# Optimization experiments

Measured on AMD Instinct MI355X. Metric: run time of the kernel, lower is better.

## Reference

```python
import jax, jax.numpy as jnp
import numpy as np

N = 20000        # total nodes in batched graph
E = 160000       # edges (avg in-degree 8)
D_IN = 512
D_OUT = 512
MAX_DEG = 10
BN_EPS = 1e-5


def setup_inputs() -> dict:
    key = jax.random.key(0)
    ks = jax.random.split(key, 8)
    feats = jax.random.normal(ks[0], (N, D_IN), dtype=jnp.float32)
    src = jax.random.randint(ks[1], (E,), 0, N)
    dst = jax.random.randint(ks[2], (E,), 0, N)
    # Wl[d], bl[d]: lins_l for degree d (d>=1); Wl[0] is never used since h==0 for deg-0 nodes.
    # Wr[0], bl[0] play the role of lin_zero_deg; Wr[d] (d>=1) are the bias-free lins_r.
    Wl = jax.random.normal(ks[3], (MAX_DEG + 1, D_IN, D_OUT), dtype=jnp.float32) * 0.02
    Wr = jax.random.normal(ks[4], (MAX_DEG + 1, D_IN, D_OUT), dtype=jnp.float32) * 0.02
    bl = jax.random.normal(ks[5], (MAX_DEG + 1, D_OUT), dtype=jnp.float32) * 0.02
    gamma = jnp.ones((D_OUT,), dtype=jnp.float32)
    beta = jnp.zeros((D_OUT,), dtype=jnp.float32)
    return {"feats": feats, "src": src, "dst": dst, "Wl": Wl, "Wr": Wr,
            "bl": bl, "gamma": gamma, "beta": beta}


def reference(feats, src, dst, Wl, Wr, bl, gamma, beta):
    # 1) neighbor sum: h[v] = sum_{(u->v) in E} feats[u]   (fn.copy_u + fn.sum)
    h = jax.ops.segment_sum(feats[src], dst, num_segments=N)  # [N, D_IN]
    # in-degrees, clamped to max_degree
    deg = jnp.clip(jax.ops.segment_sum(jnp.ones((E,), dtype=jnp.int32), dst,
                                       num_segments=N), 0, MAX_DEG)  # [N]
    # 2) degree-bucketed linears, vectorized over the 11 buckets then gathered per node.
    #    out[n] = h[n] @ Wl[deg[n]] + feats[n] @ Wr[deg[n]] + bl[deg[n]]
    #    deg==0 nodes have h==0, so this reduces to lin_zero_deg(feats) = feats@Wr[0]+bl[0].
    Hl = jnp.einsum('ni,dio->dno', h, Wl)      # [11, N, D_OUT]
    Hr = jnp.einsum('ni,dio->dno', feats, Wr)  # [11, N, D_OUT]
    out = (Hl + Hr + bl[:, None, :])[deg, jnp.arange(N)]  # [N, D_OUT]
    # 3) batchnorm (training mode: batch stats, biased variance)
    mean = out.mean(axis=0)
    var = out.var(axis=0)
    out = (out - mean) * jax.lax.rsqrt(var + BN_EPS) * gamma + beta
    # 4) max aggregation over graph with self loops (fn.copy_u + fn.max)
    self_ids = jnp.arange(N)
    src_s = jnp.concatenate([src, self_ids])
    dst_s = jnp.concatenate([dst, self_ids])
    out = jax.ops.segment_max(out[src_s], dst_s, num_segments=N)  # [N, D_OUT]
    return out
```

## Files before the change

### kernel.cpp

```cpp
#include <hip/hip_runtime.h>
#include <hip/hip_bf16.h>
#include <stdint.h>

#define N_NODES 20000
#define N_EDGES 160000
#define DIN 512
#define DOUT 512
#define NBUCKET 11
#define KDIM 1024
#define MAXTILES 168
#define BN_EPS 1e-5f
#define CAP 64
#define CAST_BLOCKS (N_NODES / 4)
#define WT_BLOCKS ((KDIM / 32) * (DOUT / 32) * NBUCKET)
#define BUCKET_BLOCKS ((N_NODES + 255) / 256)

typedef float f32x4 __attribute__((ext_vector_type(4)));
typedef __attribute__((ext_vector_type(8))) __bf16 bf16x8;

static __device__ __forceinline__ unsigned short f2bf(float f) {
    union { float f; unsigned u; } v; v.f = f;
    unsigned r = v.u + 0x7FFFu + ((v.u >> 16) & 1u);
    return (unsigned short)(r >> 16);
}
static __device__ __forceinline__ float bflo(unsigned p) {
    union { unsigned u; float f; } v; v.u = p << 16; return v.f;
}
static __device__ __forceinline__ float bfhi(unsigned p) {
    union { unsigned u; float f; } v; v.u = p & 0xFFFF0000u; return v.f;
}
static __device__ __forceinline__ unsigned packbf(float lo, float hi) {
    return (unsigned)f2bf(lo) | ((unsigned)f2bf(hi) << 16);
}

static __device__ __forceinline__ void gload_lds16(const unsigned short* g, unsigned short* l) {
    __builtin_amdgcn_global_load_lds(
        (const __attribute__((address_space(1))) unsigned int*)g,
        (__attribute__((address_space(3))) unsigned int*)l, 16, 0, 0);
}

__global__ void k_scatter(const int* __restrict__ src, const int* __restrict__ dst,
                          int* __restrict__ cursor, int* __restrict__ eidx2) {
    int e = blockIdx.x * 256 + threadIdx.x;
    if (e >= N_EDGES) return;
    int v = dst[e];
    int slot = atomicAdd(&cursor[v], 1);
    if (slot < CAP) eidx2[v * CAP + slot] = src[e];
}

__global__ __launch_bounds__(256)
void k_prep(const float* __restrict__ feats, const float* __restrict__ Wl,
            const float* __restrict__ Wr, const int* __restrict__ cursor,
            unsigned short* __restrict__ X, unsigned short* __restrict__ Wt,
            int* __restrict__ bucket_cnt, int* __restrict__ bucket_nodes) {
    int b = blockIdx.x;
    int t = threadIdx.x;
    if (b < CAST_BLOCKS) {
        int n = b * 4 + (t >> 6);
        int col = (t & 63) * 8;
        f32x4 a = *(const f32x4*)(feats + (size_t)n * DIN + col);
        f32x4 c = *(const f32x4*)(feats + (size_t)n * DIN + col + 4);
        uint4 p;
        p.x = packbf(a[0], a[1]); p.y = packbf(a[2], a[3]);
        p.z = packbf(c[0], c[1]); p.w = packbf(c[2], c[3]);
        *(uint4*)(X + (size_t)n * KDIM + DIN + col) = p;
        return;
    }
    if (b < CAST_BLOCKS + WT_BLOCKS) {
        __shared__ float tile[32][33];
        int idx = b - CAST_BLOCKS;
        int d = idx / (32 * 16);
        int rem = idx % (32 * 16);
        int k0 = (rem & 31) * 32;
        int n0 = (rem >> 5) * 32;
        int c = t & 31, r0 = t >> 5;
        const float* srcp = (k0 < DIN) ? (Wl + (size_t)d * DIN * DOUT)
                                       : (Wr + (size_t)d * DIN * DOUT - (size_t)DIN * DOUT);
        for (int rr = 0; rr < 4; ++rr) {
            int r = r0 + rr * 8;
            tile[r][c] = srcp[(size_t)(k0 + r) * DOUT + n0 + c];
        }
        __syncthreads();
        for (int rr = 0; rr < 4; ++rr) {
            int r = r0 + rr * 8;
            Wt[((size_t)d * DOUT + n0 + r) * KDIM + k0 + c] = f2bf(tile[c][r]);
        }
        return;
    }
    __shared__ int lhist[NBUCKET];
    __shared__ int lbase[NBUCKET];
    if (t < NBUCKET) lhist[t] = 0;
    __syncthreads();
    int v = (b - CAST_BLOCKS - WT_BLOCKS) * 256 + t;
    int d = -1, slot = 0;
    if (v < N_NODES) {
        d = min(cursor[v], NBUCKET - 1);
        slot = atomicAdd(&lhist[d], 1);
    }
    __syncthreads();
    if (t < NBUCKET && lhist[t] > 0) lbase[t] = atomicAdd(&bucket_cnt[t], lhist[t]);
    __syncthreads();
    if (v < N_NODES) bucket_nodes[d * N_NODES + lbase[d] + slot] = v;
}

__global__ __launch_bounds__(256)
void k_build_x(const int* __restrict__ eidx2, const int* __restrict__ cursor,
               unsigned short* __restrict__ X) {
    int n = blockIdx.x * 4 + (threadIdx.x >> 6);
    int col = (threadIdx.x & 63) * 8;
    const int* adj = eidx2 + (size_t)n * CAP;
    int e = min(cursor[n], CAP);
    float acc[8] = {0,0,0,0,0,0,0,0};
    int i = 0;
    for (; i + 3 < e; i += 4) {
        int u0 = adj[i], u1 = adj[i+1], u2 = adj[i+2], u3 = adj[i+3];
        uint4 p0 = *(const uint4*)(X + (size_t)u0 * KDIM + DIN + col);
        uint4 p1 = *(const uint4*)(X + (size_t)u1 * KDIM + DIN + col);
        uint4 p2 = *(const uint4*)(X + (size_t)u2 * KDIM + DIN + col);
        uint4 p3 = *(const uint4*)(X + (size_t)u3 * KDIM + DIN + col);
        acc[0] += bflo(p0.x) + bflo(p1.x) + bflo(p2.x) + bflo(p3.x);
        acc[1] += bfhi(p0.x) + bfhi(p1.x) + bfhi(p2.x) + bfhi(p3.x);
        acc[2] += bflo(p0.y) + bflo(p1.y) + bflo(p2.y) + bflo(p3.y);
        acc[3] += bfhi(p0.y) + bfhi(p1.y) + bfhi(p2.y) + bfhi(p3.y);
        acc[4] += bflo(p0.z) + bflo(p1.z) + bflo(p2.z) + bflo(p3.z);
        acc[5] += bfhi(p0.z) + bfhi(p1.z) + bfhi(p2.z) + bfhi(p3.z);
        acc[6] += bflo(p0.w) + bflo(p1.w) + bflo(p2.w) + bflo(p3.w);
        acc[7] += bfhi(p0.w) + bfhi(p1.w) + bfhi(p2.w) + bfhi(p3.w);
    }
    for (; i < e; ++i) {
        int u = adj[i];
        uint4 p = *(const uint4*)(X + (size_t)u * KDIM + DIN + col);
        acc[0] += bflo(p.x); acc[1] += bfhi(p.x); acc[2] += bflo(p.y); acc[3] += bfhi(p.y);
        acc[4] += bflo(p.z); acc[5] += bfhi(p.z); acc[6] += bflo(p.w); acc[7] += bfhi(p.w);
    }
    uint4 o;
    o.x = packbf(acc[0], acc[1]); o.y = packbf(acc[2], acc[3]);
    o.z = packbf(acc[4], acc[5]); o.w = packbf(acc[6], acc[7]);
    *(uint4*)(X + (size_t)n * KDIM + col) = o;
}

__global__ __launch_bounds__(256)
void k_gemm(const unsigned short* __restrict__ X, const unsigned short* __restrict__ Wt,
            const int* __restrict__ bucket_nodes, const int* __restrict__ bucket_cnt,
            const float* __restrict__ bl, unsigned short* __restrict__ out_pre,
            float* __restrict__ bn_sum, float* __restrict__ bn_sumsq) {
    int idx = blockIdx.x;
    int d = -1, m0 = 0, accum = 0, cnt = 0;
    for (int b = 0; b < NBUCKET; ++b) {
        int c = bucket_cnt[b];
        int nt = (c + 127) >> 7;
        if (d < 0 && idx < accum + nt) { d = b; m0 = (idx - accum) * 128; cnt = c; }
        accum += nt;
    }
    if (d < 0) return;
    int n0 = blockIdx.y * 128;

    __shared__ __align__(16) unsigned short As[128 * 64];
    __shared__ __align__(16) unsigned short Bs[128 * 64];
    __shared__ int ridS[128];
    __shared__ float colsum[128], colsq[128];

    int t = threadIdx.x;
    if (t < 128) {
        int gm = m0 + t;
        ridS[t] = (gm < cnt) ? bucket_nodes[d * N_NODES + gm] : -1;
        colsum[t] = 0.f; colsq[t] = 0.f;
    }
    __syncthreads();

    int lane = t & 63, w = t >> 6;
    int r = lane >> 3;
    int s = lane & 7;
    int sg = s ^ r;

    const unsigned short* gA[4];
    const unsigned short* gB[4];
    unsigned short* lA[4];
    unsigned short* lB[4];
#pragma unroll
    for (int j = 0; j < 4; ++j) {
        int row = w * 32 + j * 8 + r;
        int rid = max(ridS[row], 0);
        gA[j] = X + (size_t)rid * KDIM + sg * 8;
        gB[j] = Wt + ((size_t)d * DOUT + n0 + row) * KDIM + sg * 8;
        lA[j] = &As[(w * 32 + j * 8) * 64];
        lB[j] = &Bs[(w * 32 + j * 8) * 64];
    }

    int wm = (w & 1) * 64, wn = (w >> 1) * 64;
    int lm = lane & 15, q = lane >> 4;
    int sw = lm & 7;

    f32x4 acc[4][4];
#pragma unroll
    for (int i = 0; i < 4; ++i)
#pragma unroll
        for (int j = 0; j < 4; ++j) acc[i][j] = (f32x4){0, 0, 0, 0};

    for (int kt = 0; kt < KDIM / 64; ++kt) {
#pragma unroll
        for (int j = 0; j < 4; ++j) {
            gload_lds16(gA[j] + kt * 64, lA[j]);
            gload_lds16(gB[j] + kt * 64, lB[j]);
        }
        __syncthreads();

#pragma unroll
        for (int kk = 0; kk < 2; ++kk) {
            int slot = (kk * 4 + q) ^ sw;
            bf16x8 af[4], bfr[4];
#pragma unroll
            for (int mt = 0; mt < 4; ++mt)
                af[mt] = *(bf16x8*)&As[(wm + mt * 16 + lm) * 64 + slot * 8];
#pragma unroll
            for (int nt = 0; nt < 4; ++nt)
                bfr[nt] = *(bf16x8*)&Bs[(wn + nt * 16 + lm) * 64 + slot * 8];
#pragma unroll
            for (int mt = 0; mt < 4; ++mt)
#pragma unroll
                for (int nt = 0; nt < 4; ++nt)
                    acc[mt][nt] = __builtin_amdgcn_mfma_f32_16x16x32_bf16(af[mt], bfr[nt], acc[mt][nt], 0, 0, 0);
        }
        __syncthreads();
    }

    const float* blr = bl + d * DOUT + n0;
    float vsum[4] = {0, 0, 0, 0}, vsq[4] = {0, 0, 0, 0};
#pragma unroll
    for (int mt = 0; mt < 4; ++mt) {
#pragma unroll
        for (int rr = 0; rr < 4; ++rr) {
            int row = wm + mt * 16 + q * 4 + rr;
            int grow = ridS[row];
            if (grow < 0) continue;
            unsigned short* orow = out_pre + (size_t)grow * DOUT + n0;
#pragma unroll
            for (int nt = 0; nt < 4; ++nt) {
                int col = wn + nt * 16 + lm;
                float v = acc[mt][nt][rr] + blr[col];
                orow[col] = f2bf(v);
                vsum[nt] += v; vsq[nt] += v * v;
            }
        }
    }
#pragma unroll
    for (int nt = 0; nt < 4; ++nt) {
        vsum[nt] += __shfl_xor(vsum[nt], 16, 64);
        vsum[nt] += __shfl_xor(vsum[nt], 32, 64);
        vsq[nt]  += __shfl_xor(vsq[nt], 16, 64);
        vsq[nt]  += __shfl_xor(vsq[nt], 32, 64);
    }
    if (q == 0) {
#pragma unroll
        for (int nt = 0; nt < 4; ++nt) {
            atomicAdd(&colsum[wn + nt * 16 + lm], vsum[nt]);
            atomicAdd(&colsq[wn + nt * 16 + lm], vsq[nt]);
        }
    }
    __syncthreads();
    if (t < 128) {
        atomicAdd(&bn_sum[n0 + t], colsum[t]);
        atomicAdd(&bn_sumsq[n0 + t], colsq[t]);
    }
}

__global__ __launch_bounds__(256)
void k_max(const unsigned short* __restrict__ out_pre, const int* __restrict__ eidx2,
           const int* __restrict__ cursor, const float* __restrict__ bn_sum,
           const float* __restrict__ bn_sumsq, const float* __restrict__ gamma,
           const float* __restrict__ beta, float* __restrict__ out) {
    int n = blockIdx.x * 4 + (threadIdx.x >> 6);
    int col = (threadIdx.x & 63) * 8;
    const int* adj = eidx2 + (size_t)n * CAP;
    int e = min(cursor[n], CAP);
    float mx[8];
    {
        uint4 p = *(const uint4*)(out_pre + (size_t)n * DOUT + col);
        mx[0] = bflo(p.x); mx[1] = bfhi(p.x); mx[2] = bflo(p.y); mx[3] = bfhi(p.y);
        mx[4] = bflo(p.z); mx[5] = bfhi(p.z); mx[6] = bflo(p.w); mx[7] = bfhi(p.w);
    }
    int i = 0;
    for (; i + 3 < e; i += 4) {
        int u0 = adj[i], u1 = adj[i+1], u2 = adj[i+2], u3 = adj[i+3];
        uint4 p0 = *(const uint4*)(out_pre + (size_t)u0 * DOUT + col);
        uint4 p1 = *(const uint4*)(out_pre + (size_t)u1 * DOUT + col);
        uint4 p2 = *(const uint4*)(out_pre + (size_t)u2 * DOUT + col);
        uint4 p3 = *(const uint4*)(out_pre + (size_t)u3 * DOUT + col);
        mx[0] = fmaxf(mx[0], fmaxf(fmaxf(bflo(p0.x), bflo(p1.x)), fmaxf(bflo(p2.x), bflo(p3.x))));
        mx[1] = fmaxf(mx[1], fmaxf(fmaxf(bfhi(p0.x), bfhi(p1.x)), fmaxf(bfhi(p2.x), bfhi(p3.x))));
        mx[2] = fmaxf(mx[2], fmaxf(fmaxf(bflo(p0.y), bflo(p1.y)), fmaxf(bflo(p2.y), bflo(p3.y))));
        mx[3] = fmaxf(mx[3], fmaxf(fmaxf(bfhi(p0.y), bfhi(p1.y)), fmaxf(bfhi(p2.y), bfhi(p3.y))));
        mx[4] = fmaxf(mx[4], fmaxf(fmaxf(bflo(p0.z), bflo(p1.z)), fmaxf(bflo(p2.z), bflo(p3.z))));
        mx[5] = fmaxf(mx[5], fmaxf(fmaxf(bfhi(p0.z), bfhi(p1.z)), fmaxf(bfhi(p2.z), bfhi(p3.z))));
        mx[6] = fmaxf(mx[6], fmaxf(fmaxf(bflo(p0.w), bflo(p1.w)), fmaxf(bflo(p2.w), bflo(p3.w))));
        mx[7] = fmaxf(mx[7], fmaxf(fmaxf(bfhi(p0.w), bfhi(p1.w)), fmaxf(bfhi(p2.w), bfhi(p3.w))));
    }
    for (; i < e; ++i) {
        int u = adj[i];
        uint4 p = *(const uint4*)(out_pre + (size_t)u * DOUT + col);
        mx[0] = fmaxf(mx[0], bflo(p.x)); mx[1] = fmaxf(mx[1], bfhi(p.x));
        mx[2] = fmaxf(mx[2], bflo(p.y)); mx[3] = fmaxf(mx[3], bfhi(p.y));
        mx[4] = fmaxf(mx[4], bflo(p.z)); mx[5] = fmaxf(mx[5], bfhi(p.z));
        mx[6] = fmaxf(mx[6], bflo(p.w)); mx[7] = fmaxf(mx[7], bfhi(p.w));
    }
    const float inv_n = 1.0f / (float)N_NODES;
    f32x4 r0, r1;
#pragma unroll
    for (int jj = 0; jj < 8; ++jj) {
        int c = col + jj;
        float mean = bn_sum[c] * inv_n;
        float var = bn_sumsq[c] * inv_n - mean * mean;
        float sc = gamma[c] * rsqrtf(var + BN_EPS);
        float sh = beta[c] - mean * sc;
        float v = mx[jj] * sc + sh;
        if (jj < 4) r0[jj] = v; else r1[jj - 4] = v;
    }
    *(f32x4*)(out + (size_t)n * DOUT + col) = r0;
    *(f32x4*)(out + (size_t)n * DOUT + col + 4) = r1;
}

extern "C" void kernel_launch(void* const* d_in, const int* in_sizes, int n_in,
                              void* d_out, int out_size, void* d_ws, size_t ws_size,
                              hipStream_t stream) {
    const float* feats = (const float*)d_in[0];
    const int*   src   = (const int*)d_in[1];
    const int*   dst   = (const int*)d_in[2];
    const float* Wl    = (const float*)d_in[3];
    const float* Wr    = (const float*)d_in[4];
    const float* bl    = (const float*)d_in[5];
    const float* gamma = (const float*)d_in[6];
    const float* beta  = (const float*)d_in[7];
    float* out = (float*)d_out;

    char* ws = (char*)d_ws;
    size_t off = 0;
    auto alloc = [&](size_t bytes) -> void* {
        off = (off + 255) & ~(size_t)255;
        void* p = ws + off;
        off += bytes;
        return p;
    };

    int*   cursor     = (int*)alloc(N_NODES * 4);
    int*   bucket_cnt = (int*)alloc(16 * 4);
    float* bn_sum     = (float*)alloc(DOUT * 4);
    float* bn_sumsq   = (float*)alloc(DOUT * 4);
    size_t zbytes = off;

    int* bucket_nodes = (int*)alloc((size_t)NBUCKET * N_NODES * 4);
    int* eidx2        = (int*)alloc((size_t)N_NODES * CAP * 4);
    unsigned short* X  = (unsigned short*)alloc((size_t)N_NODES * KDIM * 2);
    unsigned short* Wt = (unsigned short*)alloc((size_t)NBUCKET * DOUT * KDIM * 2);
    unsigned short* out_pre = (unsigned short*)alloc((size_t)N_NODES * DOUT * 2);

    hipMemsetAsync(d_ws, 0, zbytes, stream);

    k_scatter<<<(N_EDGES + 255) / 256, 256, 0, stream>>>(src, dst, cursor, eidx2);
    k_prep<<<CAST_BLOCKS + WT_BLOCKS + BUCKET_BLOCKS, 256, 0, stream>>>(
        feats, Wl, Wr, cursor, X, Wt, bucket_cnt, bucket_nodes);
    k_build_x<<<N_NODES / 4, 256, 0, stream>>>(eidx2, cursor, X);
    k_gemm<<<dim3(MAXTILES, 4), 256, 0, stream>>>(
        X, Wt, bucket_nodes, bucket_cnt, bl, out_pre, bn_sum, bn_sumsq);
    k_max<<<N_NODES / 4, 256, 0, stream>>>(out_pre, eidx2, cursor, bn_sum, bn_sumsq, gamma, beta, out);
}
```

Before: 219.3 us.

## Enlarge GEMM tiles to 256x256 with double-buffered async LDS pipeline

The bucketed GEMM now uses 256x256 output tiles with 512 threads (8 waves, each computing 128x64) instead of 128x128 tiles with 256 threads. The K loop is software-pipelined: K is split into two 32-wide halves across double-buffered LDS, with global-to-LDS loads issued ahead and fine-grained vmcnt waits plus raw barriers replacing full __syncthreads. MFMA sections are wrapped with s_setprio. The aim is more reuse per loaded byte and overlap of memory with compute. The cost is a larger accumulator register footprint and more padding waste in small degree buckets, which have fewer rows than a 256-row tile.

```diff
diff --git a/kernel.cpp b/kernel.cpp
--- a/kernel.cpp
+++ b/kernel.cpp
@@ -8,7 +8,7 @@
 #define DOUT 512
 #define NBUCKET 11
 #define KDIM 1024
-#define MAXTILES 168
+#define MAXTILES 90
 #define BN_EPS 1e-5f
 #define CAP 64
 #define CAST_BLOCKS (N_NODES / 4)
@@ -139,7 +139,7 @@
     *(uint4*)(X + (size_t)n * KDIM + col) = o;
 }
 
-__global__ __launch_bounds__(256)
+__global__ __launch_bounds__(512, 2)
 void k_gemm(const unsigned short* __restrict__ X, const unsigned short* __restrict__ Wt,
             const int* __restrict__ bucket_nodes, const int* __restrict__ bucket_cnt,
             const float* __restrict__ bl, unsigned short* __restrict__ out_pre,
@@ -148,117 +148,136 @@
     int d = -1, m0 = 0, accum = 0, cnt = 0;
     for (int b = 0; b < NBUCKET; ++b) {
         int c = bucket_cnt[b];
-        int nt = (c + 127) >> 7;
-        if (d < 0 && idx < accum + nt) { d = b; m0 = (idx - accum) * 128; cnt = c; }
+        int nt = (c + 255) >> 8;
+        if (d < 0 && idx < accum + nt) { d = b; m0 = (idx - accum) * 256; cnt = c; }
         accum += nt;
     }
     if (d < 0) return;
-    int n0 = blockIdx.y * 128;
-
-    __shared__ __align__(16) unsigned short As[128 * 64];
-    __shared__ __align__(16) unsigned short Bs[128 * 64];
-    __shared__ int ridS[128];
-    __shared__ float colsum[128], colsq[128];
+    int n0 = blockIdx.y * 256;
+
+    __shared__ __align__(16) unsigned short AkLds[2][2][256 * 32];
+    __shared__ __align__(16) unsigned short BkLds[2][2][256 * 32];
+    __shared__ int ridS[256];
+    __shared__ float colsum[256], colsq[256];
 
     int t = threadIdx.x;
-    if (t < 128) {
+    if (t < 256) {
         int gm = m0 + t;
         ridS[t] = (gm < cnt) ? bucket_nodes[d * N_NODES + gm] : -1;
         colsum[t] = 0.f; colsq[t] = 0.f;
     }
     __syncthreads();
 
-    int lane = t & 63, w = t >> 6;
-    int r = lane >> 3;
-    int s = lane & 7;
-    int sg = s ^ r;
-
-    const unsigned short* gA[4];
-    const unsigned short* gB[4];
-    unsigned short* lA[4];
-    unsigned short* lB[4];
-#pragma unroll
-    for (int j = 0; j < 4; ++j) {
-        int row = w * 32 + j * 8 + r;
-        int rid = max(ridS[row], 0);
-        gA[j] = X + (size_t)rid * KDIM + sg * 8;
-        gB[j] = Wt + ((size_t)d * DOUT + n0 + row) * KDIM + sg * 8;
-        lA[j] = &As[(w * 32 + j * 8) * 64];
-        lB[j] = &Bs[(w * 32 + j * 8) * 64];
-    }
-
-    int wm = (w & 1) * 64, wn = (w >> 1) * 64;
-    int lm = lane & 15, q = lane >> 4;
-    int sw = lm & 7;
-
-    f32x4 acc[4][4];
-#pragma unroll
-    for (int i = 0; i < 4; ++i)
+    int w = t >> 6, l = t & 63;
+    int wr = w >> 2, wc = w & 3;
+    int lm = l & 15, q = l >> 4;
+
+    int srow = t >> 2;
+    int sslot = t & 3;
+    int seg = sslot ^ ((srow >> 1) & 3);
+    int ridA0 = max(ridS[srow], 0);
+    int ridA1 = max(ridS[srow + 128], 0);
+    const unsigned short* gA0 = X + (size_t)ridA0 * KDIM + seg * 8;
+    const unsigned short* gA1 = X + (size_t)ridA1 * KDIM + seg * 8;
+    const unsigned short* gB0 = Wt + ((size_t)d * DOUT + n0 + srow) * KDIM + seg * 8;
+    const unsigned short* gB1 = Wt + ((size_t)d * DOUT + n0 + srow + 128) * KDIM + seg * 8;
+
+    int swz = (lm >> 1) & 3;
+    int slotrd = ((q ^ swz) & 3) * 8;
+    int aoff = (wr * 128 + lm) * 32 + slotrd;
+    int boff = (wc * 64 + lm) * 32 + slotrd;
+
+    f32x4 acc[8][4];
+#pragma unroll
+    for (int i = 0; i < 8; ++i)
 #pragma unroll
         for (int j = 0; j < 4; ++j) acc[i][j] = (f32x4){0, 0, 0, 0};
 
+    auto STAGE = [&](int kt, int kh, int bsel) {
+        int go = kt * 64 + kh * 32;
+        gload_lds16(gA0 + go, &AkLds[bsel][kh][w * 512]);
+        gload_lds16(gA1 + go, &AkLds[bsel][kh][4096 + w * 512]);
+        gload_lds16(gB0 + go, &BkLds[bsel][kh][w * 512]);
+        gload_lds16(gB1 + go, &BkLds[bsel][kh][4096 + w * 512]);
+    };
+    auto COMPUTE = [&](int bsel, int kh) {
+        bf16x8 af[8], bfr[4];
+        const unsigned short* Ab = &AkLds[bsel][kh][0];
+        const unsigned short* Bb = &BkLds[bsel][kh][0];
+#pragma unroll
+        for (int mf = 0; mf < 8; ++mf)
+            af[mf] = *(const bf16x8*)&Ab[aoff + mf * 512];
+#pragma unroll
+        for (int nf = 0; nf < 4; ++nf)
+            bfr[nf] = *(const bf16x8*)&Bb[boff + nf * 512];
+        __builtin_amdgcn_s_setprio(1);
+#pragma unroll
+        for (int mf = 0; mf < 8; ++mf)
+#pragma unroll
+            for (int nf = 0; nf < 4; ++nf)
+                acc[mf][nf] = __builtin_amdgcn_mfma_f32_16x16x32_bf16(af[mf], bfr[nf], acc[mf][nf], 0, 0, 0);
+        __builtin_amdgcn_s_setprio(0);
+    };
+
+    STAGE(0, 0, 0);
+    STAGE(0, 1, 0);
+    STAGE(1, 0, 1);
+    asm volatile("s_waitcnt vmcnt(8)" ::: "memory");
+    __builtin_amdgcn_s_barrier();
+    asm volatile("" ::: "memory");
+
+#pragma unroll 1
     for (int kt = 0; kt < KDIM / 64; ++kt) {
-#pragma unroll
-        for (int j = 0; j < 4; ++j) {
-            gload_lds16(gA[j] + kt * 64, lA[j]);
-            gload_lds16(gB[j] + kt * 64, lB[j]);
-        }
-        __syncthreads();
-
-#pragma unroll
-        for (int kk = 0; kk < 2; ++kk) {
-            int slot = (kk * 4 + q) ^ sw;
-            bf16x8 af[4], bfr[4];
-#pragma unroll
-            for (int mt = 0; mt < 4; ++mt)
-                af[mt] = *(bf16x8*)&As[(wm + mt * 16 + lm) * 64 + slot * 8];
-#pragma unroll
-            for (int nt = 0; nt < 4; ++nt)
-                bfr[nt] = *(bf16x8*)&Bs[(wn + nt * 16 + lm) * 64 + slot * 8];
-#pragma unroll
-            for (int mt = 0; mt < 4; ++mt)
-#pragma unroll
-                for (int nt = 0; nt < 4; ++nt)
-                    acc[mt][nt] = __builtin_amdgcn_mfma_f32_16x16x32_bf16(af[mt], bfr[nt], acc[mt][nt], 0, 0, 0);
-        }
-        __syncthreads();
+        int buf = kt & 1;
+        if (kt < 15) STAGE(kt + 1, 1, buf ^ 1);
+        COMPUTE(buf, 0);
+        if (kt < 15) asm volatile("s_waitcnt vmcnt(8)" ::: "memory");
+        else         asm volatile("s_waitcnt vmcnt(0)" ::: "memory");
+        __builtin_amdgcn_s_barrier();
+        asm volatile("" ::: "memory");
+        if (kt < 14) STAGE(kt + 2, 0, buf);
+        COMPUTE(buf, 1);
+        if (kt < 14)       asm volatile("s_waitcnt vmcnt(8)" ::: "memory");
+        else if (kt == 14) asm volatile("s_waitcnt vmcnt(4)" ::: "memory");
+        __builtin_amdgcn_s_barrier();
+        asm volatile("" ::: "memory");
     }
 
     const float* blr = bl + d * DOUT + n0;
     float vsum[4] = {0, 0, 0, 0}, vsq[4] = {0, 0, 0, 0};
 #pragma unroll
-    for (int mt = 0; mt < 4; ++mt) {
+    for (int mf = 0; mf < 8; ++mf) {
 #pragma unroll
         for (int rr = 0; rr < 4; ++rr) {
-            int row = wm + mt * 16 + q * 4 + rr;
+            int row = wr * 128 + mf * 16 + q * 4 + rr;
             int grow = ridS[row];
             if (grow < 0) continue;
             unsigned short* orow = out_pre + (size_t)grow * DOUT + n0;
 #pragma unroll
-            for (int nt = 0; nt < 4; ++nt) {
-                int col = wn + nt * 16 + lm;
-                float v = acc[mt][nt][rr] + blr[col];
+            for (int nf = 0; nf < 4; ++nf) {
+                int col = wc * 64 + nf * 16 + lm;
+                float v = acc[mf][nf][rr] + blr[col];
                 orow[col] = f2bf(v);
-                vsum[nt] += v; vsq[nt] += v * v;
+                vsum[nf] += v; vsq[nf] += v * v;
             }
         }
     }
 #pragma unroll
-    for (int nt = 0; nt < 4; ++nt) {
-        vsum[nt] += __shfl_xor(vsum[nt], 16, 64);
-        vsum[nt] += __shfl_xor(vsum[nt], 32, 64);
-        vsq[nt]  += __shfl_xor(vsq[nt], 16, 64);
-        vsq[nt]  += __shfl_xor(vsq[nt], 32, 64);
+    for (int nf = 0; nf < 4; ++nf) {
+        vsum[nf] += __shfl_xor(vsum[nf], 16, 64);
+        vsum[nf] += __shfl_xor(vsum[nf], 32, 64);
+        vsq[nf]  += __shfl_xor(vsq[nf], 16, 64);
+        vsq[nf]  += __shfl_xor(vsq[nf], 32, 64);
     }
     if (q == 0) {
 #pragma unroll
-        for (int nt = 0; nt < 4; ++nt) {
-            atomicAdd(&colsum[wn + nt * 16 + lm], vsum[nt]);
-            atomicAdd(&colsq[wn + nt * 16 + lm], vsq[nt]);
+        for (int nf = 0; nf < 4; ++nf) {
+            atomicAdd(&colsum[wc * 64 + nf * 16 + lm], vsum[nf]);
+            atomicAdd(&colsq[wc * 64 + nf * 16 + lm], vsq[nf]);
         }
     }
     __syncthreads();
-    if (t < 128) {
+    if (t < 256) {
         atomicAdd(&bn_sum[n0 + t], colsum[t]);
         atomicAdd(&bn_sumsq[n0 + t], colsq[t]);
     }
@@ -359,7 +378,7 @@
     k_prep<<<CAST_BLOCKS + WT_BLOCKS + BUCKET_BLOCKS, 256, 0, stream>>>(
         feats, Wl, Wr, cursor, X, Wt, bucket_cnt, bucket_nodes);
     k_build_x<<<N_NODES / 4, 256, 0, stream>>>(eidx2, cursor, X);
-    k_gemm<<<dim3(MAXTILES, 4), 256, 0, stream>>>(
+    k_gemm<<<dim3(MAXTILES, 2), 512, 0, stream>>>(
         X, Wt, bucket_nodes, bucket_cnt, bl, out_pre, bn_sum, bn_sumsq);
     k_max<<<N_NODES / 4, 256, 0, stream>>>(out_pre, eidx2, cursor, bn_sum, bn_sumsq, gamma, beta, out);
 }
```

Measured after the change: 228.4 us. 4.1% more time.
